# Performance work log

Hardware: AMD Instinct MI355X
Metric: run time of the kernel (lower is better)

Reference implementation:

```python
import jax, jax.numpy as jnp
import numpy as np
from jax import lax

B, C, H, W = 4, 24, 128, 128
R = 7
NUM_CLASSES = 6
MAX_STEPS = 8


def _conv(x, w, b, pad):
    y = lax.conv_general_dilated(x, w, (1, 1), [(pad, pad), (pad, pad)],
                                 dimension_numbers=("NCHW", "OIHW", "NCHW"))
    return y + b[None, :, None, None]


def setup_inputs() -> dict:
    key = jax.random.key(0)
    ks = jax.random.split(key, 16)
    s = 0.05
    inp = {
        "depth_latent": jax.random.normal(ks[0], (B, C, H, W), jnp.float32),
        "texture_features": jax.random.normal(ks[1], (B, 3, H, W), jnp.float32),
        "class_labels": jax.random.randint(ks[2], (B,), 0, NUM_CLASSES),
        # texture_encoder
        "w_te1": jax.random.normal(ks[3], (64, 3, 3, 3), jnp.float32) * s,
        "b_te1": jnp.zeros((64,), jnp.float32),
        "w_te2": jax.random.normal(ks[4], (128, 64, 3, 3), jnp.float32) * s,
        "b_te2": jnp.zeros((128,), jnp.float32),
        # class embedding [num_classes, 128]
        "emb": jax.random.normal(ks[5], (NUM_CLASSES, 128), jnp.float32) * s,
        # fusion_layer: Conv2d(256,256,3) -> Conv2d(256, C*R*R, 1)
        "w_f1": jax.random.normal(ks[6], (256, 256, 3, 3), jnp.float32) * s,
        "b_f1": jnp.zeros((256,), jnp.float32),
        "w_f2": jax.random.normal(ks[7], (C * R * R, 256, 1, 1), jnp.float32) * s,
        "b_f2": jnp.zeros((C * R * R,), jnp.float32),
        # class_gate: Conv2d(128,64,3) -> Conv2d(64,num_classes,1)
        "w_g1": jax.random.normal(ks[8], (64, 128, 3, 3), jnp.float32) * s,
        "b_g1": jnp.zeros((64,), jnp.float32),
        "w_g2": jax.random.normal(ks[9], (NUM_CLASSES, 64, 1, 1), jnp.float32) * s,
        "b_g2": jnp.zeros((NUM_CLASSES,), jnp.float32),
        "class_intensity": jnp.ones((1, NUM_CLASSES, 1, 1), jnp.float32),
    }
    return inp


def _forward(depth_latent, texture_features, class_labels,
             w_te1, b_te1, w_te2, b_te2, emb,
             w_f1, b_f1, w_f2, b_f2,
             w_g1, b_g1, w_g2, b_g2, class_intensity):
    pad = R // 2
    # texture encoder
    tex = jax.nn.relu(_conv(texture_features, w_te1, b_te1, 1))
    tex = jax.nn.relu(_conv(tex, w_te2, b_te2, 1))  # [B,128,H,W]

    # 1-D integer class label path
    class_cond = jax.nn.one_hot(class_labels, NUM_CLASSES, dtype=jnp.float32)[:, :, None, None]  # [B,K,1,1]
    class_emb = emb[class_labels][:, :, None, None]  # [B,128,1,1]

    gate = jax.nn.sigmoid(_conv(jax.nn.relu(_conv(tex, w_g1, b_g1, 1)), w_g2, b_g2, 0))
    class_gate = gate * class_cond  # [B,K,H,W]

    fused = jnp.concatenate([tex, jnp.broadcast_to(class_emb, (tex.shape[0], 128, H, W))], axis=1)
    weights = _conv(jax.nn.relu(_conv(fused, w_f1, b_f1, 1)), w_f2, b_f2, 0)
    weights = weights.reshape(-1, C, R * R, H, W)

    intensity_map = (class_gate * class_intensity).sum(axis=1, keepdims=True)  # [B,1,H,W]
    weights = weights * intensity_map[:, :, None]  # [B,C,R*R,H,W]
    weights = jax.nn.softmax(weights, axis=2)

    def diffusion_step(lat):
        p = jnp.pad(lat, ((0, 0), (0, 0), (pad, pad), (pad, pad)), mode="edge")
        # unfold order: kernel row-major (i*R + j)
        windows = jnp.stack([p[:, :, i:i + H, j:j + W]
                             for i in range(R) for j in range(R)], axis=2)
        return (windows * weights).sum(axis=2)

    enhanced = lax.fori_loop(0, MAX_STEPS, lambda _, lat: diffusion_step(lat), depth_latent)

    condition_map = intensity_map * class_gate.sum(axis=1, keepdims=True)
    return enhanced, class_gate, condition_map


def reference(depth_latent, texture_features, class_labels,
              w_te1, b_te1, w_te2, b_te2, emb,
              w_f1, b_f1, w_f2, b_f2,
              w_g1, b_g1, w_g2, b_g2, class_intensity):
    return _forward(depth_latent, texture_features, class_labels,
                    w_te1, b_te1, w_te2, b_te2, emb,
                    w_f1, b_f1, w_f2, b_f2,
                    w_g1, b_g1, w_g2, b_g2, class_intensity)
```

## Files before the change

kernel.cpp:

```cpp
#include <hip/hip_runtime.h>
#include <hip/hip_bf16.h>
#include <stdint.h>

#define DINL __device__ __forceinline__

DINL float bf2f(__hip_bfloat16 v) { return __bfloat162float(v); }
DINL __hip_bfloat16 f2bf(float v) { return __float2bfloat16(v); }
DINL float bflo(unsigned int u) { return __uint_as_float(u << 16); }
DINL float bfhi(unsigned int u) { return __uint_as_float(u & 0xffff0000u); }

DINL float loadf(float v) { return v; }
DINL float loadf(__hip_bfloat16 v) { return __bfloat162float(v); }

typedef __attribute__((ext_vector_type(8))) short bf16x8;
typedef __attribute__((ext_vector_type(4))) float f32x4;

DINL void gld_lds16(const void* g, void* l) {
  __builtin_amdgcn_global_load_lds(
      (const __attribute__((address_space(1))) unsigned int*)g,
      (__attribute__((address_space(3))) unsigned int*)l, 16, 0, 0);
}

#define O_WTE1 0
#define O_WG2  1792
#define O_SS   2304
#define O_INT  11520
#define BO_W2B   308224u
#define BO_TE2B 1094656u
#define BO_WG1B 1242112u
#define BO_WF1B 1389568u
#define BO_TEX  4194304u
#define BO_F1   20971520u
#define BO_PING 54525952u
#define BO_PONG 60817408u
#define BO_W    67108864u
#define BO_T1   BO_W

__global__ __launch_bounds__(256) void prep_kernel(
    const float* __restrict__ w_te1, const float* __restrict__ w_te2,
    const float* __restrict__ w_g1,  const float* __restrict__ w_f1,
    const float* __restrict__ w_f2,  const float* __restrict__ w_g2,
    const float* __restrict__ emb,   const int* __restrict__ labels,
    float* __restrict__ wsf)
{
  const int gid = blockIdx.x * 256 + threadIdx.x;
  const int stride = gridDim.x * 256;
  const int A0 = 1728, A1 = A0 + 393216, A2 = A1 + 73728, A3 = A2 + 73728,
            A4 = A3 + 294912, A5 = A4 + 384;
  __hip_bfloat16* w2b  = (__hip_bfloat16*)((char*)wsf + BO_W2B);
  __hip_bfloat16* te2b = (__hip_bfloat16*)((char*)wsf + BO_TE2B);
  __hip_bfloat16* g1b  = (__hip_bfloat16*)((char*)wsf + BO_WG1B);
  __hip_bfloat16* f1b  = (__hip_bfloat16*)((char*)wsf + BO_WF1B);
  for (int i = gid; i < A5; i += stride) {
    if (i < A0) {
      int s = i; int o = s / 27; int r = s - o * 27; int ic = r / 9; int t = r - ic * 9;
      wsf[O_WTE1 + (((o >> 5) * 3 + ic) * 9 + t) * 32 + (o & 31)] = w_te1[s];
    } else if (i < A1) {
      int s = i - A0;
      int j = s & 7; int lane = (s >> 3) & 63; int ks = (s >> 9) & 7;
      int mt = (s >> 12) & 3; int c = s >> 14;
      int tap = mt * 16 + (lane & 15);
      int k = ks * 32 + (lane >> 4) * 8 + j;
      float v = (tap < 49) ? w_f2[(c * 49 + tap) * 256 + k] : 0.f;
      w2b[s] = f2bf(v);
    } else if (i < A2) {
      int s = i - A1;
      int k = s & 31; int n = (s >> 5) & 63; int u = s >> 11;
      int t = u % 9; int v = u / 9; int kc = v & 1; int ocg = v >> 1;
      te2b[s] = f2bf(w_te2[((ocg * 64 + n) * 64 + kc * 32 + k) * 9 + t]);
    } else if (i < A3) {
      int s = i - A2;
      int k = s & 31; int n = (s >> 5) & 63; int u = s >> 11;
      int t = u % 9; int kc = u / 9;
      g1b[s] = f2bf(w_g1[(n * 128 + kc * 32 + k) * 9 + t]);
    } else if (i < A4) {
      int s = i - A3;
      int k = s & 31; int n = (s >> 5) & 63; int u = s >> 11;
      int t = u % 9; int v = u / 9; int kc = v & 3; int ocg = v >> 2;
      f1b[s] = f2bf(w_f1[((ocg * 64 + n) * 256 + kc * 32 + k) * 9 + t]);
    } else {
      int s = i - A4;
      wsf[O_WG2 + s] = w_g2[s];
    }
  }
  if (gid < 16384) {
    const int g = gid >> 4, slot = gid & 15;
    const int b = g >> 8, o = g & 255;
    const int lab = labels[b];
    float St[9];
#pragma unroll
    for (int t = 0; t < 9; ++t) St[t] = 0.f;
#pragma unroll 2
    for (int k = 0; k < 8; ++k) {
      const int i = slot * 8 + k;
      const float e = emb[lab * 128 + i];
      const float* wr = w_f1 + (size_t)(o * 256 + 128 + i) * 9;
#pragma unroll
      for (int t = 0; t < 9; ++t) St[t] += wr[t] * e;
    }
#pragma unroll
    for (int d = 1; d < 16; d <<= 1)
#pragma unroll
      for (int t = 0; t < 9; ++t) St[t] += __shfl_xor(St[t], d, 64);
    if (slot == 0) {
#pragma unroll
      for (int ch = 0; ch < 3; ++ch)
#pragma unroll
        for (int cw = 0; cw < 3; ++cw) {
          float sum = 0.f;
#pragma unroll
          for (int t = 0; t < 9; ++t) {
            int kh = t / 3, kw = t - kh * 3;
            bool ok = !(ch == 0 && kh == 0) && !(ch == 2 && kh == 2) &&
                      !(cw == 0 && kw == 0) && !(cw == 2 && kw == 2);
            if (ok) sum += St[t];
          }
          wsf[O_SS + g * 9 + ch * 3 + cw] = sum;
        }
    }
  }
}

template<typename TIn, int ICH, bool PIXMAJOR>
__global__ __launch_bounds__(256, 2) void conv3x3_kernel(
    const TIn* __restrict__ in, const float* __restrict__ wf,
    const float* __restrict__ bias,
    __hip_bfloat16* __restrict__ out, const int och_total)
{
  constexpr int CH = (ICH < 16) ? ICH : 16;
  constexpr int NCHUNK = ICH / CH;
  __shared__ TIn sIn[CH][18][20];
  const int tid = threadIdx.x;
  const int b = blockIdx.z;
  const int ob = blockIdx.y;
  const int och0 = ob * 32;
  const int tileY = blockIdx.x >> 3, tileX = blockIdx.x & 7;
  const int ty = tid >> 4, tx = tid & 15;
  const int h = tileY * 16 + ty, w = tileX * 16 + tx;
  const int h0 = tileY * 16 - 1, w0 = tileX * 16 - 1;

  float acc[32];
#pragma unroll
  for (int o = 0; o < 32; ++o) acc[o] = bias[och0 + o];

  for (int cc = 0; cc < NCHUNK; ++cc) {
    if (cc) __syncthreads();
    for (int e = tid; e < CH * 324; e += 256) {
      int ic = e / 324, r = e - ic * 324;
      int y = r / 18, x = r - y * 18;
      int gh = h0 + y, gw = w0 + x;
      TIn v = TIn(0.f);
      if ((unsigned)gh < 128u && (unsigned)gw < 128u)
        v = in[((b * ICH + cc * CH + ic) << 14) + (gh << 7) + gw];
      sIn[ic][y][x] = v;
    }
    __syncthreads();
#pragma unroll 1
    for (int ic = 0; ic < CH; ++ic) {
      const float* wrow = wf + (ob * ICH + cc * CH + ic) * 288;
#pragma unroll
      for (int t = 0; t < 9; ++t) {
        const int kh = t / 3, kw = t - kh * 3;
        const float v = loadf(sIn[ic][ty + kh][tx + kw]);
#pragma unroll
        for (int o = 0; o < 32; ++o)
          acc[o] = fmaf(wrow[t * 32 + o], v, acc[o]);
      }
    }
  }

  const int pix = (h << 7) + w;
  if constexpr (!PIXMAJOR) {
#pragma unroll
    for (int o = 0; o < 32; ++o)
      out[((b * och_total + och0 + o) << 14) + pix] = f2bf(fmaxf(acc[o], 0.f));
  } else {
    union { uint4 u4[4]; __hip_bfloat16 hh[32]; } pk;
#pragma unroll
    for (int o = 0; o < 32; ++o) pk.hh[o] = f2bf(fmaxf(acc[o], 0.f));
    uint4* dst = reinterpret_cast<uint4*>(out + ((size_t)(b << 14) + pix) * och_total + och0);
#pragma unroll
    for (int i = 0; i < 4; ++i) dst[i] = pk.u4[i];
  }
}

template<int ICH, bool ADD_SS, bool GATE>
__global__ __launch_bounds__(256, 2) void conv3x3_mfma_kernel(
    const __hip_bfloat16* __restrict__ in, const __hip_bfloat16* __restrict__ wb,
    const float* __restrict__ bias, const float* __restrict__ SS,
    __hip_bfloat16* __restrict__ out, const int och_total,
    const float* __restrict__ wg2, const float* __restrict__ b_g2,
    const int* __restrict__ labels, const float* __restrict__ ci,
    float* __restrict__ out_cg, float* __restrict__ out_cond,
    float* __restrict__ inten)
{
  constexpr int NKC = ICH / 32;
  __shared__ __hip_bfloat16 smem[36000];
#define SHX(pos, k) smem[(pos) * 40 + (k)]
#define SWX(t, n, k) smem[12960 + (((t) * 64 + (n)) * 40) + (k)]
  const int tid = threadIdx.x, b = blockIdx.z, ocg = blockIdx.y;
  const int tileY = blockIdx.x >> 3, tileX = blockIdx.x & 7;
  const int h0 = tileY * 16 - 1, w0 = tileX * 16 - 1;
  const int wave = tid >> 6, lane = tid & 63, m16 = lane & 15, quad = lane >> 4;

  f32x4 acc[4][4];
#pragma unroll
  for (int i = 0; i < 4; ++i)
#pragma unroll
    for (int j = 0; j < 4; ++j) acc[i][j] = f32x4{0.f, 0.f, 0.f, 0.f};

  for (int kc = 0; kc < NKC; ++kc) {
    if (kc) __syncthreads();
    for (int e = tid; e < 1296; e += 256) {
      int pos = e >> 2, q = e & 3;
      int y = pos / 18, x = pos - y * 18;
      int gh = h0 + y, gw = w0 + x;
      uint4 v = uint4{0u, 0u, 0u, 0u};
      if ((unsigned)gh < 128u && (unsigned)gw < 128u)
        v = *(const uint4*)(in + ((size_t)((b << 14) + (gh << 7) + gw)) * ICH + kc * 32 + q * 8);
      *(uint4*)&SHX(pos, q * 8) = v;
    }
    const uint4* wsrc = (const uint4*)(wb + ((size_t)(ocg * NKC + kc)) * 9 * 64 * 32);
    for (int e = tid; e < 2304; e += 256) {
      int q = e & 3, n = (e >> 2) & 63, t = e >> 8;
      *(uint4*)&SWX(t, n, q * 8) = wsrc[e];
    }
    __syncthreads();
#pragma unroll
    for (int t = 0; t < 9; ++t) {
      const int dy = t / 3, dx = t - dy * 3;
      bf16x8 bfr[4];
#pragma unroll
      for (int nt = 0; nt < 4; ++nt)
        bfr[nt] = *(const bf16x8*)&SWX(t, nt * 16 + m16, quad * 8);
#pragma unroll
      for (int mi = 0; mi < 4; ++mi) {
        const int py = wave * 4 + mi;
        const bf16x8 afr = *(const bf16x8*)&SHX((py + dy) * 18 + dx + m16, quad * 8);
#pragma unroll
        for (int nt = 0; nt < 4; ++nt)
          acc[mi][nt] = __builtin_amdgcn_mfma_f32_16x16x32_bf16(afr, bfr[nt], acc[mi][nt], 0, 0, 0);
      }
    }
  }

  float bv[4];
#pragma unroll
  for (int nt = 0; nt < 4; ++nt) bv[nt] = bias[ocg * 64 + nt * 16 + m16];

  if constexpr (GATE) {
    __syncthreads();
    __hip_bfloat16* sG = smem;
#pragma unroll
    for (int mi = 0; mi < 4; ++mi)
#pragma unroll
      for (int nt = 0; nt < 4; ++nt) {
        const int och = nt * 16 + m16;
#pragma unroll
        for (int r = 0; r < 4; ++r) {
          const int p = (wave * 4 + mi) * 16 + quad * 4 + r;
          sG[p * 68 + och] = f2bf(fmaxf(acc[mi][nt][r] + bv[nt], 0.f));
        }
      }
    __syncthreads();
    const int p = tid;
    float a6[6];
#pragma unroll
    for (int k = 0; k < 6; ++k) a6[k] = b_g2[k];
#pragma unroll
    for (int i8 = 0; i8 < 8; ++i8) {
      const bf16x8 v8 = *(const bf16x8*)&sG[p * 68 + i8 * 8];
#pragma unroll
      for (int j = 0; j < 8; ++j) {
        const float v = bf2f(((const __hip_bfloat16*)&v8)[j]);
#pragma unroll
        for (int k = 0; k < 6; ++k)
          a6[k] = fmaf(wg2[k * 64 + i8 * 8 + j], v, a6[k]);
      }
    }
    const int lab = labels[b];
    float gate[6], gl = 0.f;
#pragma unroll
    for (int k = 0; k < 6; ++k) {
      gate[k] = 1.f / (1.f + __expf(-a6[k]));
      gl = (k == lab) ? gate[k] : gl;
    }
    const float civ = ci[lab];
    const float it = gl * civ;
    const int h = tileY * 16 + (p >> 4), w = tileX * 16 + (p & 15);
    const int pix = (h << 7) + w;
#pragma unroll
    for (int k = 0; k < 6; ++k)
      out_cg[((b * 6 + k) << 14) + pix] = (k == lab) ? gate[k] : 0.f;
    inten[(b << 14) + pix] = it;
    out_cond[(b << 14) + pix] = it * gl;
    return;
  }

#pragma unroll
  for (int mi = 0; mi < 4; ++mi) {
    const int py = wave * 4 + mi;
    const int h = tileY * 16 + py;
    const int chc = (h == 0) ? 0 : ((h == 127) ? 2 : 1);
#pragma unroll
    for (int nt = 0; nt < 4; ++nt) {
      float sr0 = 0.f, sr1 = 0.f, sr2 = 0.f;
      if constexpr (ADD_SS) {
        const float* sp = SS + ((size_t)(b << 8) + (ocg * 64 + nt * 16 + m16)) * 9;
        sr0 = sp[chc * 3 + 0]; sr1 = sp[chc * 3 + 1]; sr2 = sp[chc * 3 + 2];
      }
      const int och = ocg * 64 + nt * 16 + m16;
#pragma unroll
      for (int r = 0; r < 4; ++r) {
        const int px = quad * 4 + r;
        const int w = tileX * 16 + px;
        float v = acc[mi][nt][r] + bv[nt];
        if constexpr (ADD_SS)
          v += (w == 0) ? sr0 : ((w == 127) ? sr2 : sr1);
        v = fmaxf(v, 0.f);
        out[((size_t)((b << 14) + (h << 7) + w)) * och_total + och] = f2bf(v);
      }
    }
  }
#undef SHX
#undef SWX
}

__global__ __launch_bounds__(256, 3) void gemm_softmax_kernel(
    const __hip_bfloat16* __restrict__ f1, const __hip_bfloat16* __restrict__ w2b,
    const float* __restrict__ b_f2, const float* __restrict__ inten,
    __hip_bfloat16* __restrict__ wout)
{
  __shared__ __hip_bfloat16 sW[2][8192];
  __shared__ __hip_bfloat16 sT[49][136];
  const int tid = threadIdx.x;
  const int pix0 = blockIdx.x * 128;
  const int c0 = blockIdx.y * 8;
  const int wave = tid >> 6, lane = tid & 63;
  const int n16 = lane & 15, quad = lane >> 4;
  const int p0 = pix0 + wave * 16 + n16;
  const int p1 = p0 + 64;

  bf16x8 bfr0[8], bfr1[8];
#pragma unroll
  for (int ks = 0; ks < 8; ++ks) {
    bfr0[ks] = *(const bf16x8*)(f1 + (size_t)p0 * 256 + ks * 32 + quad * 8);
    bfr1[ks] = *(const bf16x8*)(f1 + (size_t)p1 * 256 + ks * 32 + quad * 8);
  }

  const float s0v = inten[p0], s1v = inten[p1];
  const int ob = pix0 >> 14, op = pix0 & 16383;

#define W2U(u) ((const uint4*)(w2b + ((((size_t)c0 + ((u) >> 1)) * 4 + (((u) & 1) << 1)) << 12)))

  {
    const uint4* s0 = W2U(0);
    uint4* d0 = (uint4*)&sW[0][0];
#pragma unroll
    for (int j = 0; j < 4; ++j)
      gld_lds16(s0 + tid + j * 256, d0 + tid + j * 256);
  }
  __syncthreads();

#pragma unroll 1
  for (int cl = 0; cl < 8; ++cl) {
    const int c = c0 + cl;
    f32x4 ac0[4], ac1[4];
#pragma unroll
    for (int mt = 0; mt < 4; ++mt) { ac0[mt] = f32x4{0.f,0.f,0.f,0.f}; ac1[mt] = f32x4{0.f,0.f,0.f,0.f}; }

#pragma unroll
    for (int h = 0; h < 2; ++h) {
      const int u = cl * 2 + h;
      {
        const uint4* sn = W2U(u < 15 ? u + 1 : 15);
        uint4* dn = (uint4*)&sW[(u + 1) & 1][0];
#pragma unroll
        for (int j = 0; j < 4; ++j)
          gld_lds16(sn + tid + j * 256, dn + tid + j * 256);
      }

      const __hip_bfloat16* bufp = &sW[u & 1][0];
#pragma unroll
      for (int ks = 0; ks < 8; ++ks) {
        const bf16x8 a0 = *(const bf16x8*)(bufp + ((ks) * 64 + lane) * 8);
        const bf16x8 a1 = *(const bf16x8*)(bufp + ((8 + ks) * 64 + lane) * 8);
        ac0[h * 2 + 0] = __builtin_amdgcn_mfma_f32_16x16x32_bf16(a0, bfr0[ks], ac0[h * 2 + 0], 0, 0, 0);
        ac1[h * 2 + 0] = __builtin_amdgcn_mfma_f32_16x16x32_bf16(a0, bfr1[ks], ac1[h * 2 + 0], 0, 0, 0);
        ac0[h * 2 + 1] = __builtin_amdgcn_mfma_f32_16x16x32_bf16(a1, bfr0[ks], ac0[h * 2 + 1], 0, 0, 0);
        ac1[h * 2 + 1] = __builtin_amdgcn_mfma_f32_16x16x32_bf16(a1, bfr1[ks], ac1[h * 2 + 1], 0, 0, 0);
      }
      __syncthreads();
    }

    const float b48 = b_f2[c * 49 + 48];
#pragma unroll
    for (int g = 0; g < 2; ++g) {
      f32x4* ac = g ? ac1 : ac0;
      const float s = g ? s1v : s0v;
      float mx = -3.4e38f;
#pragma unroll
      for (int mt = 0; mt < 3; ++mt)
#pragma unroll
        for (int r = 0; r < 4; ++r) {
          const float lv = (ac[mt][r] + b_f2[c * 49 + mt * 16 + quad * 4 + r]) * s;
          ac[mt][r] = lv;
          mx = fmaxf(mx, lv);
        }
      const float v48 = (ac[3][0] + b48) * s;
      if (quad == 0) mx = fmaxf(mx, v48);
      mx = fmaxf(mx, __shfl_xor(mx, 16, 64));
      mx = fmaxf(mx, __shfl_xor(mx, 32, 64));
      float sum = 0.f;
#pragma unroll
      for (int mt = 0; mt < 3; ++mt)
#pragma unroll
        for (int r = 0; r < 4; ++r) {
          const float e = __expf(ac[mt][r] - mx);
          ac[mt][r] = e;
          sum += e;
        }
      const float e48 = (quad == 0) ? __expf(v48 - mx) : 0.f;
      sum += e48;
      sum += __shfl_xor(sum, 16, 64);
      sum += __shfl_xor(sum, 32, 64);
      const float rs = 1.f / sum;

      const int px = wave * 16 + n16 + g * 64;
#pragma unroll
      for (int mt = 0; mt < 3; ++mt)
#pragma unroll
        for (int r = 0; r < 4; ++r)
          sT[mt * 16 + quad * 4 + r][px] = f2bf(ac[mt][r] * rs);
      if (quad == 0) sT[48][px] = f2bf(e48 * rs);
    }
    __syncthreads();

    __hip_bfloat16* wob = wout + (((size_t)(ob * 24 + c) * 49) << 14) + op;
    for (int e = tid; e < 784; e += 256) {
      const int tap = e >> 4, qq = e & 15;
      *(uint4*)(wob + ((size_t)tap << 14) + qq * 8) = *(const uint4*)&sT[tap][qq * 8];
    }
  }
#undef W2U
}

__global__ __launch_bounds__(256) void diff_kernel(
    const float* __restrict__ lin, const __hip_bfloat16* __restrict__ wts,
    float* __restrict__ lout)
{
  __shared__ float sT[22][136];
  const int bc = blockIdx.y;
  const int h0 = blockIdx.x * 16;
  const int tid = threadIdx.x;
  for (int e = tid; e < 22 * 134; e += 256) {
    int y = e / 134, x = e - y * 134;
    int gh = min(max(h0 - 3 + y, 0), 127), gw = min(max(x - 3, 0), 127);
    sT[y][x] = lin[(bc << 14) + (gh << 7) + gw];
  }
  __syncthreads();
  const int tx8 = (tid & 15) * 8;
  const int ty = tid >> 4;
  const int h = h0 + ty;
  const __hip_bfloat16* wp = wts + (((size_t)bc * 49) << 14) + (h << 7) + tx8;
  float a[8];
#pragma unroll
  for (int j = 0; j < 8; ++j) a[j] = 0.f;
#pragma unroll
  for (int kh = 0; kh < 7; ++kh) {
    const float* row = &sT[ty + kh][tx8];
    float r[16];
    *(f32x4*)&r[0]  = *(const f32x4*)(row);
    *(f32x4*)&r[4]  = *(const f32x4*)(row + 4);
    *(f32x4*)&r[8]  = *(const f32x4*)(row + 8);
    *(f32x4*)&r[12] = *(const f32x4*)(row + 12);
#pragma unroll
    for (int kw = 0; kw < 7; ++kw) {
      const int t = kh * 7 + kw;
      const uint4 wq = *(const uint4*)(wp + ((size_t)t << 14));
      a[0] = fmaf(bflo(wq.x), r[kw + 0], a[0]);
      a[1] = fmaf(bfhi(wq.x), r[kw + 1], a[1]);
      a[2] = fmaf(bflo(wq.y), r[kw + 2], a[2]);
      a[3] = fmaf(bfhi(wq.y), r[kw + 3], a[3]);
      a[4] = fmaf(bflo(wq.z), r[kw + 4], a[4]);
      a[5] = fmaf(bfhi(wq.z), r[kw + 5], a[5]);
      a[6] = fmaf(bflo(wq.w), r[kw + 6], a[6]);
      a[7] = fmaf(bfhi(wq.w), r[kw + 7], a[7]);
    }
  }
  float* dst = lout + (bc << 14) + (h << 7) + tx8;
  *(f32x4*)dst       = f32x4{a[0], a[1], a[2], a[3]};
  *(f32x4*)(dst + 4) = f32x4{a[4], a[5], a[6], a[7]};
}

extern "C" void kernel_launch(void* const* d_in, const int* in_sizes, int n_in,
                              void* d_out, int out_size, void* d_ws, size_t ws_size,
                              hipStream_t stream)
{
  const float* depth = (const float*)d_in[0];
  const float* texf  = (const float*)d_in[1];
  const int*   labels= (const int*)d_in[2];
  const float* w_te1 = (const float*)d_in[3];
  const float* b_te1 = (const float*)d_in[4];
  const float* w_te2 = (const float*)d_in[5];
  const float* b_te2 = (const float*)d_in[6];
  const float* emb   = (const float*)d_in[7];
  const float* w_f1  = (const float*)d_in[8];
  const float* b_f1  = (const float*)d_in[9];
  const float* w_f2  = (const float*)d_in[10];
  const float* b_f2  = (const float*)d_in[11];
  const float* w_g1  = (const float*)d_in[12];
  const float* b_g1  = (const float*)d_in[13];
  const float* w_g2  = (const float*)d_in[14];
  const float* b_g2  = (const float*)d_in[15];
  const float* ci    = (const float*)d_in[16];

  char*  ws  = (char*)d_ws;
  float* wsf = (float*)d_ws;
  __hip_bfloat16* w2bf  = (__hip_bfloat16*)(ws + BO_W2B);
  __hip_bfloat16* te2bf = (__hip_bfloat16*)(ws + BO_TE2B);
  __hip_bfloat16* g1bf  = (__hip_bfloat16*)(ws + BO_WG1B);
  __hip_bfloat16* f1bf  = (__hip_bfloat16*)(ws + BO_WF1B);
  __hip_bfloat16* tex   = (__hip_bfloat16*)(ws + BO_TEX);
  __hip_bfloat16* f1    = (__hip_bfloat16*)(ws + BO_F1);
  float* ping           = (float*)(ws + BO_PING);
  float* pong           = (float*)(ws + BO_PONG);
  __hip_bfloat16* wts   = (__hip_bfloat16*)(ws + BO_W);
  __hip_bfloat16* t1    = (__hip_bfloat16*)(ws + BO_T1);

  float* out      = (float*)d_out;
  float* out_enh  = out;
  float* out_cg   = out + 1572864;
  float* out_cond = out + 1966080;

  prep_kernel<<<512, 256, 0, stream>>>(w_te1, w_te2, w_g1, w_f1, w_f2, w_g2, emb, labels, wsf);
  conv3x3_kernel<float, 3, true><<<dim3(64, 2, 4), 256, 0, stream>>>(texf, wsf + O_WTE1, b_te1, t1, 64);
  conv3x3_mfma_kernel<64,  false, false><<<dim3(64, 2, 4), 256, 0, stream>>>(
      t1, te2bf, b_te2, nullptr, tex, 128,
      nullptr, nullptr, nullptr, nullptr, nullptr, nullptr, nullptr);
  conv3x3_mfma_kernel<128, false, true><<<dim3(64, 1, 4), 256, 0, stream>>>(
      tex, g1bf, b_g1, nullptr, nullptr, 64,
      wsf + O_WG2, b_g2, labels, ci, out_cg, out_cond, wsf + O_INT);
  conv3x3_mfma_kernel<128, true, false><<<dim3(64, 4, 4), 256, 0, stream>>>(
      tex, f1bf, b_f1, wsf + O_SS, f1, 256,
      nullptr, nullptr, nullptr, nullptr, nullptr, nullptr, nullptr);
  gemm_softmax_kernel<<<dim3(512, 3), 256, 0, stream>>>(f1, w2bf, b_f2, wsf + O_INT, wts);

  dim3 dgrid(8, 96);
  diff_kernel<<<dgrid, 256, 0, stream>>>(depth, wts, ping);
  diff_kernel<<<dgrid, 256, 0, stream>>>(ping, wts, pong);
  diff_kernel<<<dgrid, 256, 0, stream>>>(pong, wts, ping);
  diff_kernel<<<dgrid, 256, 0, stream>>>(ping, wts, pong);
  diff_kernel<<<dgrid, 256, 0, stream>>>(pong, wts, ping);
  diff_kernel<<<dgrid, 256, 0, stream>>>(ping, wts, pong);
  diff_kernel<<<dgrid, 256, 0, stream>>>(pong, wts, ping);
  diff_kernel<<<dgrid, 256, 0, stream>>>(ping, wts, out_enh);
}
```

Baseline: 494.1 us.

## Double pixel tile in gemm-softmax and halve diffusion block rows

```diff
diff --git a/kernel.cpp b/kernel.cpp
--- a/kernel.cpp
+++ b/kernel.cpp
@@ -326,29 +326,31 @@
 #undef SWX
 }
 
-__global__ __launch_bounds__(256, 3) void gemm_softmax_kernel(
+__global__ __launch_bounds__(256, 2) void gemm_softmax_kernel(
     const __hip_bfloat16* __restrict__ f1, const __hip_bfloat16* __restrict__ w2b,
     const float* __restrict__ b_f2, const float* __restrict__ inten,
     __hip_bfloat16* __restrict__ wout)
 {
   __shared__ __hip_bfloat16 sW[2][8192];
-  __shared__ __hip_bfloat16 sT[49][136];
+  __shared__ __hip_bfloat16 sT[49][272];
   const int tid = threadIdx.x;
-  const int pix0 = blockIdx.x * 128;
+  const int pix0 = blockIdx.x * 256;
   const int c0 = blockIdx.y * 8;
   const int wave = tid >> 6, lane = tid & 63;
   const int n16 = lane & 15, quad = lane >> 4;
-  const int p0 = pix0 + wave * 16 + n16;
-  const int p1 = p0 + 64;
-
-  bf16x8 bfr0[8], bfr1[8];
-#pragma unroll
-  for (int ks = 0; ks < 8; ++ks) {
-    bfr0[ks] = *(const bf16x8*)(f1 + (size_t)p0 * 256 + ks * 32 + quad * 8);
-    bfr1[ks] = *(const bf16x8*)(f1 + (size_t)p1 * 256 + ks * 32 + quad * 8);
-  }
-
-  const float s0v = inten[p0], s1v = inten[p1];
+  const int pb = pix0 + wave * 16 + n16;
+
+  bf16x8 bfr[4][8];
+  float sv[4];
+#pragma unroll
+  for (int g = 0; g < 4; ++g) {
+    const int p = pb + g * 64;
+#pragma unroll
+    for (int ks = 0; ks < 8; ++ks)
+      bfr[g][ks] = *(const bf16x8*)(f1 + (size_t)p * 256 + ks * 32 + quad * 8);
+    sv[g] = inten[p];
+  }
+
   const int ob = pix0 >> 14, op = pix0 & 16383;
 
 #define W2U(u) ((const uint4*)(w2b + ((((size_t)c0 + ((u) >> 1)) * 4 + (((u) & 1) << 1)) << 12)))
@@ -365,9 +367,11 @@
 #pragma unroll 1
   for (int cl = 0; cl < 8; ++cl) {
     const int c = c0 + cl;
-    f32x4 ac0[4], ac1[4];
-#pragma unroll
-    for (int mt = 0; mt < 4; ++mt) { ac0[mt] = f32x4{0.f,0.f,0.f,0.f}; ac1[mt] = f32x4{0.f,0.f,0.f,0.f}; }
+    f32x4 ac[4][4];
+#pragma unroll
+    for (int g = 0; g < 4; ++g)
+#pragma unroll
+      for (int mt = 0; mt < 4; ++mt) ac[g][mt] = f32x4{0.f,0.f,0.f,0.f};
 
 #pragma unroll
     for (int h = 0; h < 2; ++h) {
@@ -385,29 +389,30 @@
       for (int ks = 0; ks < 8; ++ks) {
         const bf16x8 a0 = *(const bf16x8*)(bufp + ((ks) * 64 + lane) * 8);
         const bf16x8 a1 = *(const bf16x8*)(bufp + ((8 + ks) * 64 + lane) * 8);
-        ac0[h * 2 + 0] = __builtin_amdgcn_mfma_f32_16x16x32_bf16(a0, bfr0[ks], ac0[h * 2 + 0], 0, 0, 0);
-        ac1[h * 2 + 0] = __builtin_amdgcn_mfma_f32_16x16x32_bf16(a0, bfr1[ks], ac1[h * 2 + 0], 0, 0, 0);
-        ac0[h * 2 + 1] = __builtin_amdgcn_mfma_f32_16x16x32_bf16(a1, bfr0[ks], ac0[h * 2 + 1], 0, 0, 0);
-        ac1[h * 2 + 1] = __builtin_amdgcn_mfma_f32_16x16x32_bf16(a1, bfr1[ks], ac1[h * 2 + 1], 0, 0, 0);
+#pragma unroll
+        for (int g = 0; g < 4; ++g) {
+          ac[g][h * 2 + 0] = __builtin_amdgcn_mfma_f32_16x16x32_bf16(a0, bfr[g][ks], ac[g][h * 2 + 0], 0, 0, 0);
+          ac[g][h * 2 + 1] = __builtin_amdgcn_mfma_f32_16x16x32_bf16(a1, bfr[g][ks], ac[g][h * 2 + 1], 0, 0, 0);
+        }
       }
       __syncthreads();
     }
 
     const float b48 = b_f2[c * 49 + 48];
 #pragma unroll
-    for (int g = 0; g < 2; ++g) {
-      f32x4* ac = g ? ac1 : ac0;
-      const float s = g ? s1v : s0v;
+    for (int g = 0; g < 4; ++g) {
+      f32x4* acg = ac[g];
+      const float s = sv[g];
       float mx = -3.4e38f;
 #pragma unroll
       for (int mt = 0; mt < 3; ++mt)
 #pragma unroll
         for (int r = 0; r < 4; ++r) {
-          const float lv = (ac[mt][r] + b_f2[c * 49 + mt * 16 + quad * 4 + r]) * s;
-          ac[mt][r] = lv;
+          const float lv = (acg[mt][r] + b_f2[c * 49 + mt * 16 + quad * 4 + r]) * s;
+          acg[mt][r] = lv;
           mx = fmaxf(mx, lv);
         }
-      const float v48 = (ac[3][0] + b48) * s;
+      const float v48 = (acg[3][0] + b48) * s;
       if (quad == 0) mx = fmaxf(mx, v48);
       mx = fmaxf(mx, __shfl_xor(mx, 16, 64));
       mx = fmaxf(mx, __shfl_xor(mx, 32, 64));
@@ -416,8 +421,8 @@
       for (int mt = 0; mt < 3; ++mt)
 #pragma unroll
         for (int r = 0; r < 4; ++r) {
-          const float e = __expf(ac[mt][r] - mx);
-          ac[mt][r] = e;
+          const float e = __expf(acg[mt][r] - mx);
+          acg[mt][r] = e;
           sum += e;
         }
       const float e48 = (quad == 0) ? __expf(v48 - mx) : 0.f;
@@ -431,29 +436,29 @@
       for (int mt = 0; mt < 3; ++mt)
 #pragma unroll
         for (int r = 0; r < 4; ++r)
-          sT[mt * 16 + quad * 4 + r][px] = f2bf(ac[mt][r] * rs);
+          sT[mt * 16 + quad * 4 + r][px] = f2bf(acg[mt][r] * rs);
       if (quad == 0) sT[48][px] = f2bf(e48 * rs);
     }
     __syncthreads();
 
     __hip_bfloat16* wob = wout + (((size_t)(ob * 24 + c) * 49) << 14) + op;
-    for (int e = tid; e < 784; e += 256) {
-      const int tap = e >> 4, qq = e & 15;
+    for (int e = tid; e < 1568; e += 256) {
+      const int tap = e >> 5, qq = e & 31;
       *(uint4*)(wob + ((size_t)tap << 14) + qq * 8) = *(const uint4*)&sT[tap][qq * 8];
     }
   }
 #undef W2U
 }
 
-__global__ __launch_bounds__(256) void diff_kernel(
+__global__ __launch_bounds__(128) void diff_kernel(
     const float* __restrict__ lin, const __hip_bfloat16* __restrict__ wts,
     float* __restrict__ lout)
 {
-  __shared__ float sT[22][136];
+  __shared__ float sT[14][136];
   const int bc = blockIdx.y;
-  const int h0 = blockIdx.x * 16;
+  const int h0 = blockIdx.x * 8;
   const int tid = threadIdx.x;
-  for (int e = tid; e < 22 * 134; e += 256) {
+  for (int e = tid; e < 14 * 134; e += 128) {
     int y = e / 134, x = e - y * 134;
     int gh = min(max(h0 - 3 + y, 0), 127), gw = min(max(x - 3, 0), 127);
     sT[y][x] = lin[(bc << 14) + (gh << 7) + gw];
@@ -544,15 +549,15 @@
   conv3x3_mfma_kernel<128, true, false><<<dim3(64, 4, 4), 256, 0, stream>>>(
       tex, f1bf, b_f1, wsf + O_SS, f1, 256,
       nullptr, nullptr, nullptr, nullptr, nullptr, nullptr, nullptr);
-  gemm_softmax_kernel<<<dim3(512, 3), 256, 0, stream>>>(f1, w2bf, b_f2, wsf + O_INT, wts);
-
-  dim3 dgrid(8, 96);
-  diff_kernel<<<dgrid, 256, 0, stream>>>(depth, wts, ping);
-  diff_kernel<<<dgrid, 256, 0, stream>>>(ping, wts, pong);
-  diff_kernel<<<dgrid, 256, 0, stream>>>(pong, wts, ping);
-  diff_kernel<<<dgrid, 256, 0, stream>>>(ping, wts, pong);
-  diff_kernel<<<dgrid, 256, 0, stream>>>(pong, wts, ping);
-  diff_kernel<<<dgrid, 256, 0, stream>>>(ping, wts, pong);
-  diff_kernel<<<dgrid, 256, 0, stream>>>(pong, wts, ping);
-  diff_kernel<<<dgrid, 256, 0, stream>>>(ping, wts, out_enh);
-}
+  gemm_softmax_kernel<<<dim3(256, 3), 256, 0, stream>>>(f1, w2bf, b_f2, wsf + O_INT, wts);
+
+  dim3 dgrid(16, 96);
+  diff_kernel<<<dgrid, 128, 0, stream>>>(depth, wts, ping);
+  diff_kernel<<<dgrid, 128, 0, stream>>>(ping, wts, pong);
+  diff_kernel<<<dgrid, 128, 0, stream>>>(pong, wts, ping);
+  diff_kernel<<<dgrid, 128, 0, stream>>>(ping, wts, pong);
+  diff_kernel<<<dgrid, 128, 0, stream>>>(pong, wts, ping);
+  diff_kernel<<<dgrid, 128, 0, stream>>>(ping, wts, pong);
+  diff_kernel<<<dgrid, 128, 0, stream>>>(pong, wts, ping);
+  diff_kernel<<<dgrid, 128, 0, stream>>>(ping, wts, out_enh);
+}
```

After: 517.0 us. 1.05x slower.
